# Kernel optimization log

Measured on AMD Instinct MI355X. Metric: run time of the kernel, lower is better.

## Reference

```python
import jax, jax.numpy as jnp
import numpy as np

N_CELLS_PER_SIDE = 16
MAX_K = 32
N_HEADS = 8
CHUNK = 128

_NEIGHBOR_OFFSETS = jnp.array([[-1, -1], [-1, 0], [-1, 1], [0, -1], [0, 0], [0, 1], [1, -1], [1, 0], [1, 1]], dtype=jnp.int32)


def cell_lookup(query_pos, cell_map, pos_min, pos_range):
    B, S, _ = query_pos.shape
    mpc = cell_map.shape[1]
    normalized = (query_pos - pos_min) / pos_range
    cell_xy = jnp.clip((normalized * N_CELLS_PER_SIDE).astype(jnp.int32), 0, N_CELLS_PER_SIDE - 1)
    nb = jnp.clip(cell_xy[:, :, None, :] + _NEIGHBOR_OFFSETS[None, None, :, :], 0, N_CELLS_PER_SIDE - 1)
    nidx = nb[..., 0] * N_CELLS_PER_SIDE + nb[..., 1]
    cand = cell_map[nidx].reshape(B, S, 9 * mpc)
    valid = cand >= 0
    return jnp.where(valid, cand, 0), valid


def threshold_gate(scores, tau, max_k):
    raw = scores - tau
    gate = jnp.where(raw > 0, raw, 1e-8 * jnp.exp(raw))
    eg = jnp.exp(gate) - 1.0
    k = min(max_k, scores.shape[-1])
    tv, _ = jax.lax.top_k(eg, k)
    eg = jnp.where(eg >= tv[:, :, -1:], eg, 0.0)
    gs = eg.sum(axis=-1, keepdims=True) + 1e-8
    strength = jnp.tanh(eg.max(axis=-1, keepdims=True))
    return eg / gs * strength


def setup_inputs() -> dict:
    key = jax.random.key(0)
    ks = jax.random.split(key, 16)
    B, S, D, N, P = 2, 1024, 512, 4096, 2
    n_cells, mpc = N_CELLS_PER_SIDE ** 2, 32
    return {
        "x": jax.random.normal(ks[0], (B, S, D), jnp.float32),
        "qk_pos": jax.random.uniform(ks[1], (B, S, P), jnp.float32),
        "v_pos": jax.random.uniform(ks[2], (B, S, P), jnp.float32),
        "tau_Q": jax.random.uniform(ks[3], (B, S, 1), jnp.float32),
        "tau_K": jax.random.uniform(ks[4], (B, S, 1), jnp.float32),
        "tau_V": jax.random.uniform(ks[5], (B, S, 1), jnp.float32),
        "qk_neurons": jax.random.normal(ks[6], (N, D), jnp.float32) / np.float32(np.sqrt(D)),
        "v_neurons": jax.random.normal(ks[7], (N, D), jnp.float32) / np.float32(np.sqrt(D)),
        "npos_qk": jax.random.uniform(ks[8], (N, P), jnp.float32),
        "npos_v": jax.random.uniform(ks[9], (N, P), jnp.float32),
        "cell_map_qk": jax.random.randint(ks[10], (n_cells, mpc), 0, N, jnp.int32),
        "cell_map_v": jax.random.randint(ks[11], (n_cells, mpc), 0, N, jnp.int32),
        "pos_min": jnp.zeros((P,), jnp.float32),
        "pos_range": jnp.ones((P,), jnp.float32),
        "expand_O": jax.random.normal(ks[12], (D, D), jnp.float32) * 0.02,
    }


def reference(x, qk_pos, v_pos, tau_Q, tau_K, tau_V, qk_neurons, v_neurons, npos_qk, npos_v, cell_map_qk, cell_map_v, pos_min, pos_range, expand_O):
    B, S, D = x.shape
    # full-sequence spatial cell lookup (small int tensors)
    ci_qk, m_qk = cell_lookup(qk_pos, cell_map_qk, pos_min, pos_range)
    ci_v, m_v = cell_lookup(v_pos, cell_map_v, pos_min, pos_range)
    ci_qk = jax.lax.stop_gradient(ci_qk)
    ci_v = jax.lax.stop_gradient(ci_v)
    nc = S // CHUNK  # S chosen divisible by CHUNK (no padding path needed)

    def chunks(a):
        return a.reshape(B, nc, CHUNK, *a.shape[2:]).swapaxes(0, 1)

    inp = tuple(map(chunks, (x, qk_pos, v_pos, tau_Q, tau_K, tau_V, ci_qk, m_qk, ci_v, m_v)))

    def step(carry, c):
        x_c, qkp, vp, tq, tk, tv, i_qk, mk, i_v, mv = c
        cand_qk = qk_neurons[i_qk]  # [B,C,n_cand,D]
        cand_v = v_neurons[i_v]
        act_qk = jnp.einsum('bsd,bsnd->bsn', x_c, cand_qk)
        act_v = jnp.einsum('bsd,bsnd->bsn', x_c, cand_v)
        s_qk = jnp.where(mk, act_qk, -1e9)
        s_v = jnp.where(mv, act_v, -1e9)
        gQ = threshold_gate(s_qk, tq, MAX_K)
        gK = threshold_gate(s_qk, tk, MAX_K)
        gV = threshold_gate(s_v, tv, MAX_K)
        Q_c = jnp.einsum('bsn,bsnd->bsd', act_qk * gQ * mk, cand_qk)
        K_c = jnp.einsum('bsn,bsnd->bsd', act_qk * gK * mk, cand_qk)
        V_c = jnp.einsum('bsn,bsnd->bsd', act_v * gV * mv, cand_v)
        pd_qk = jnp.sum((qkp[:, :, None, :] - npos_qk[i_qk]) ** 2, axis=-1)
        pl_qk = (jax.lax.stop_gradient(gQ) * pd_qk * mk).sum() / (mk.sum() + 1e-8)
        pd_v = jnp.sum((vp[:, :, None, :] - npos_v[i_v]) ** 2, axis=-1)
        pl_v = (jax.lax.stop_gradient(gV) * pd_v * mv).sum() / (mv.sum() + 1e-8)
        return carry, (Q_c, K_c, V_c, pl_qk + pl_v)

    _, (Qs, Ks, Vs, pls) = jax.lax.scan(step, 0, inp)

    def merge(a):
        return a.swapaxes(0, 1).reshape(B, S, D)

    Q, K, V = merge(Qs), merge(Ks), merge(Vs)
    pos_loss = pls.mean()  # == sum / n_chunks

    dh = D // N_HEADS
    Qh = Q.reshape(B, S, N_HEADS, dh).transpose(0, 2, 1, 3)
    Kh = K.reshape(B, S, N_HEADS, dh).transpose(0, 2, 1, 3)
    Vh = V.reshape(B, S, N_HEADS, dh).transpose(0, 2, 1, 3)
    scores = jnp.einsum('bhsd,bhtd->bhst', Qh, Kh) / jnp.sqrt(jnp.float32(dh))
    causal = jnp.tril(jnp.ones((S, S), dtype=jnp.bool_))
    scores = jnp.where(causal, scores, jnp.finfo(scores.dtype).min)
    attn = jax.nn.softmax(scores, axis=-1)
    out = jnp.einsum('bhst,bhtd->bhsd', attn, Vh)
    out = out.transpose(0, 2, 1, 3).reshape(B, S, D)
    out = out @ expand_O
    return out, pos_loss
```

## Files before the change

### kernel.cpp

```cpp
#include <hip/hip_runtime.h>
#include <math.h>

#define B_ 2
#define S_ 1024
#define D_ 512
#define N_ 4096
#define H_ 8
#define DH_ 64
#define NCAND 288
#define TOPK 32
#define NTOK (B_*S_)
#define NG8 512

#define NROWS 16384
#define NSLOT_BH 8704
#define NSLOTS (16*NSLOT_BH)

__device__ __forceinline__ float wave_sum(float v) {
    #pragma unroll
    for (int o = 32; o; o >>= 1) v += __shfl_xor(v, o);
    return v;
}
__device__ __forceinline__ float wave_max(float v) {
    #pragma unroll
    for (int o = 32; o; o >>= 1) v = fmaxf(v, __shfl_xor(v, o));
    return v;
}
__device__ __forceinline__ void fma4(float4& a, float s, const float4 b) {
    a.x += s * b.x; a.y += s * b.y; a.z += s * b.z; a.w += s * b.w;
}

__global__ __launch_bounds__(1024) void sort_tokens_kernel(
    const float* __restrict__ qk_pos, const float* __restrict__ v_pos,
    const float* __restrict__ pos_min, const float* __restrict__ pos_range,
    int* __restrict__ order_qk, int* __restrict__ order_v,
    int2* __restrict__ desc_qk, int2* __restrict__ desc_v)
{
    __shared__ int hist[256], tmp[256], offs[256], startc[256], gcnt[256];
    const int t = threadIdx.x;
    const int pass = blockIdx.x;
    const float pm0 = pos_min[0], pm1 = pos_min[1];
    const float pr0 = pos_range[0], pr1 = pos_range[1];
    const float* pos = pass ? v_pos : qk_pos;
    int* order = pass ? order_v : order_qk;
    int2* desc = pass ? desc_v : desc_qk;
    if (t < NG8) desc[t] = make_int2(0, 0);
    if (t < 256) hist[t] = 0;
    __syncthreads();
    int cell[2];
    #pragma unroll
    for (int k = 0; k < 2; k++) {
        int tok = t + k * 1024;
        float p0 = pos[tok * 2], p1 = pos[tok * 2 + 1];
        int cx = min(max((int)((p0 - pm0) / pr0 * 16.f), 0), 15);
        int cy = min(max((int)((p1 - pm1) / pr1 * 16.f), 0), 15);
        cell[k] = cx * 16 + cy;
        atomicAdd(&hist[cell[k]], 1);
    }
    __syncthreads();
    if (t < 256) tmp[t] = hist[t];
    __syncthreads();
    for (int d = 1; d < 256; d <<= 1) {
        int v = 0;
        if (t < 256 && t >= d) v = tmp[t - d];
        __syncthreads();
        if (t < 256) tmp[t] += v;
        __syncthreads();
    }
    if (t < 256) {
        startc[t] = tmp[t] - hist[t];
        offs[t]   = startc[t];
        gcnt[t]   = (hist[t] + 7) >> 3;
    }
    __syncthreads();
    #pragma unroll
    for (int k = 0; k < 2; k++) {
        int tok = t + k * 1024;
        int p = atomicAdd(&offs[cell[k]], 1);
        order[p] = tok;
    }
    __syncthreads();
    if (t < 256) tmp[t] = gcnt[t];
    __syncthreads();
    for (int d = 1; d < 256; d <<= 1) {
        int v = 0;
        if (t < 256 && t >= d) v = tmp[t - d];
        __syncthreads();
        if (t < 256) tmp[t] += v;
        __syncthreads();
    }
    if (t < 256) {
        int g0 = tmp[t] - gcnt[t];
        for (int k = 0; k < gcnt[t]; k++)
            desc[g0 + k] = make_int2(startc[t] + 8 * k, min(8, hist[t] - 8 * k));
    }
}

__device__ __forceinline__ int rank_topk(const float* __restrict__ actRow,
                                         int* __restrict__ ciRow, int lane) {
    unsigned ej[5];
    #pragma unroll
    for (int k = 0; k < 5; k++) {
        int j = lane + 64 * k;
        float f = (j < NCAND) ? actRow[j] : -1e30f;
        unsigned uu = __float_as_uint(f);
        ej[k] = (uu & 0x80000000u) ? ~uu : (uu | 0x80000000u);
    }
    unsigned T = 0u;
    for (int bit = 31; bit >= 0; bit--) {
        const unsigned cand = T | (1u << bit);
        int c = 0;
        #pragma unroll
        for (int k = 0; k < 5; k++)
            c += __popcll(__ballot(ej[k] >= cand));
        if (c >= TOPK) T = cand;
    }
    int base = 0;
    const unsigned long long below = (lane == 0) ? 0ull : (~0ull >> (64 - lane));
    #pragma unroll
    for (int k = 0; k < 5; k++) {
        const unsigned long long mk2 = __ballot(ej[k] >= T);
        if (ej[k] >= T) {
            int pos = base + __popcll(mk2 & below);
            ciRow[pos] = lane + 64 * k;
        }
        base += __popcll(mk2);
    }
    return base;
}

__global__ __launch_bounds__(256) void qkv_fused(
    const int2* __restrict__ desc_qk, const int* __restrict__ order_qk,
    const int2* __restrict__ desc_v,  const int* __restrict__ order_v,
    const float* __restrict__ x,
    const float* __restrict__ qk_pos, const float* __restrict__ v_pos,
    const float* __restrict__ tauQ, const float* __restrict__ tauK,
    const float* __restrict__ tauV,
    const float* __restrict__ qk_neurons, const float* __restrict__ v_neurons,
    const float* __restrict__ npos_qk, const float* __restrict__ npos_v,
    const int* __restrict__ cm_qk, const int* __restrict__ cm_v,
    const float* __restrict__ pos_min, const float* __restrict__ pos_range,
    float* __restrict__ Q, float* __restrict__ K, float* __restrict__ V,
    float* __restrict__ posacc)
{
    const int bid = blockIdx.x;
    const int role = bid & 1;
    const int gid = bid >> 1;
    const int2 dsc = role ? desc_v[gid] : desc_qk[gid];
    const int gstart = dsc.x, count = dsc.y;
    if (count == 0) return;

    const int*   order   = role ? order_v   : order_qk;
    const float* pose    = role ? v_pos     : qk_pos;
    const float* neurons = role ? v_neurons : qk_neurons;
    const float* npos    = role ? npos_v    : npos_qk;
    const int*   cmap    = role ? cm_v      : cm_qk;

    __shared__ int   idx[NCAND];
    __shared__ float msk[NCAND];
    __shared__ float act[8][NCAND];
    __shared__ int   ci[8][NCAND];
    __shared__ float cw1[8][NCAND], cw2[8][NCAND];
    __shared__ int   toks[8];

    const int t = threadIdx.x, wid = t >> 6, lane = t & 63;
    const int sub = lane & 15, grp = lane >> 4;
    if (t < 8) toks[t] = order[gstart + min(t, count - 1)];
    __syncthreads();
    const int token0 = toks[0];

    const float pm0 = pos_min[0], pm1 = pos_min[1];
    const float pr0 = pos_range[0], pr1 = pos_range[1];
    {
        const float p0 = pose[token0 * 2], p1 = pose[token0 * 2 + 1];
        const int cx = min(max((int)((p0 - pm0) / pr0 * 16.f), 0), 15);
        const int cy = min(max((int)((p1 - pm1) / pr1 * 16.f), 0), 15);
        for (int c = t; c < NCAND; c += 256) {
            int o = c >> 5, ms = c & 31;
            int nx = min(max(cx + o / 3 - 1, 0), 15), ny = min(max(cy + o % 3 - 1, 0), 15);
            int cand = cmap[(nx * 16 + ny) * 32 + ms];
            idx[c] = cand >= 0 ? cand : 0;
            msk[c] = cand >= 0 ? 1.f : 0.f;
        }
    }
    __syncthreads();

    const int tokA = 2 * grp, tokB = 2 * grp + 1;
    float4 xr0[8], xr1[8];
    {
        const float4* xp0 = (const float4*)(x + (size_t)toks[tokA] * D_);
        const float4* xp1 = (const float4*)(x + (size_t)toks[tokB] * D_);
        #pragma unroll
        for (int k = 0; k < 8; k++) {
            xr0[k] = xp0[k * 16 + sub];
            xr1[k] = xp1[k * 16 + sub];
        }
    }

    #define LOADROW(buf, c) do { \
        const float4* rp_ = (const float4*)(neurons + (size_t)idx[c] * D_); \
        _Pragma("unroll") \
        for (int k_ = 0; k_ < 8; k_++) buf[k_] = rp_[k_ * 16 + sub]; \
    } while (0)
    #define DOTSTORE(buf, c) do { \
        float f0_ = 0.f, f1_ = 0.f; \
        _Pragma("unroll") \
        for (int k_ = 0; k_ < 8; k_++) { \
            f0_ += xr0[k_].x*buf[k_].x + xr0[k_].y*buf[k_].y + xr0[k_].z*buf[k_].z + xr0[k_].w*buf[k_].w; \
            f1_ += xr1[k_].x*buf[k_].x + xr1[k_].y*buf[k_].y + xr1[k_].z*buf[k_].z + xr1[k_].w*buf[k_].w; \
        } \
        _Pragma("unroll") \
        for (int o_ = 1; o_ <= 8; o_ <<= 1) { \
            f0_ += __shfl_xor(f0_, o_); \
            f1_ += __shfl_xor(f1_, o_); \
        } \
        if (sub == 0) { \
            const float mv_ = msk[c]; \
            act[tokA][c] = (mv_ != 0.f) ? f0_ : -1e9f; \
            act[tokB][c] = (mv_ != 0.f) ? f1_ : -1e9f; \
        } \
    } while (0)

    {
        const int cb = wid * 72;
        float4 bufA[8], bufB[8];
        LOADROW(bufA, cb);
        for (int u = 0; u < 72; u += 2) {
            LOADROW(bufB, cb + u + 1);
            DOTSTORE(bufA, cb + u);
            if (u + 2 < 72) LOADROW(bufA, cb + u + 2);
            DOTSTORE(bufB, cb + u + 1);
        }
    }
    __syncthreads();

    float cmv = 0.f;
    for (int c = lane; c < NCAND; c += 64) cmv += msk[c];
    const float cm = wave_sum(cmv);

    int n0 = 0, n1 = 0;
    if (2 * wid < count)     n0 = rank_topk(act[2 * wid],     ci[2 * wid],     lane);
    if (2 * wid + 1 < count) n1 = rank_topk(act[2 * wid + 1], ci[2 * wid + 1], lane);

    if (role == 0) {
        #pragma unroll
        for (int i = 0; i < 2; i++) {
            const int tk = 2 * wid + i;
            if (tk >= count) continue;
            const int n = i ? n1 : n0;
            const int token = toks[tk];
            const float tq = tauQ[token], tkk = tauK[token];
            float sQ = 0.f, sK = 0.f, mQ = 0.f, mK = 0.f;
            for (int p = lane; p < n; p += 64) {
                float s = act[tk][ci[tk][p]];
                float rq = s - tq;
                float gq = (rq > 0.f) ? rq : 1e-8f * __expf(rq);
                float egq = __expf(gq) - 1.f;
                float rk = s - tkk;
                float gk = (rk > 0.f) ? rk : 1e-8f * __expf(rk);
                float egk = __expf(gk) - 1.f;
                cw1[tk][p] = egq; cw2[tk][p] = egk;
                sQ += egq; sK += egk;
                mQ = fmaxf(mQ, egq); mK = fmaxf(mK, egk);
            }
            sQ = wave_sum(sQ); mQ = wave_max(mQ);
            sK = wave_sum(sK); mK = wave_max(mK);
            const float scQ = tanhf(mQ) / (sQ + 1e-8f);
            const float scK = tanhf(mK) / (sK + 1e-8f);

            const float qp0 = pose[token * 2], qp1 = pose[token * 2 + 1];
            float plq = 0.f;
            for (int p = lane; p < n; p += 64) {
                int e = ci[tk][p];
                int id = idx[e];
                float m = msk[e], a = act[tk][e];
                float gq = cw1[tk][p] * scQ;
                cw1[tk][p] = a * gq * m;
                cw2[tk][p] = a * cw2[tk][p] * scK * m;
                ci[tk][p] = id;
                float d0 = qp0 - npos[id * 2], d1 = qp1 - npos[id * 2 + 1];
                plq += gq * (d0 * d0 + d1 * d1) * m;
            }
            plq = wave_sum(plq);
            if (lane == 0) {
                int chunk = (token & 1023) >> 7;
                atomicAdd(&posacc[chunk], plq);
                atomicAdd(&posacc[8 + chunk], cm);
            }

            float4 qa0 = {0,0,0,0}, qa1 = {0,0,0,0};
            float4 ka0 = {0,0,0,0}, ka1 = {0,0,0,0};
            int p = 0;
            for (; p + 1 < n; p += 2) {
                const float* rA = neurons + (size_t)ci[tk][p] * D_ + lane * 8;
                const float* rB = neurons + (size_t)ci[tk][p + 1] * D_ + lane * 8;
                const float4 A0 = *(const float4*)rA;
                const float4 A1 = *(const float4*)(rA + 4);
                const float4 B0 = *(const float4*)rB;
                const float4 B1 = *(const float4*)(rB + 4);
                const float wA = cw1[tk][p], bA = cw2[tk][p];
                const float wB = cw1[tk][p + 1], bB = cw2[tk][p + 1];
                fma4(qa0, wA, A0); fma4(qa0, wB, B0);
                fma4(qa1, wA, A1); fma4(qa1, wB, B1);
                fma4(ka0, bA, A0); fma4(ka0, bB, B0);
                fma4(ka1, bA, A1); fma4(ka1, bB, B1);
            }
            if (p < n) {
                const float* rA = neurons + (size_t)ci[tk][p] * D_ + lane * 8;
                const float4 A0 = *(const float4*)rA;
                const float4 A1 = *(const float4*)(rA + 4);
                const float wA = cw1[tk][p], bA = cw2[tk][p];
                fma4(qa0, wA, A0); fma4(qa1, wA, A1);
                fma4(ka0, bA, A0); fma4(ka1, bA, A1);
            }
            *(float4*)(Q + (size_t)token * D_ + lane * 8)     = qa0;
            *(float4*)(Q + (size_t)token * D_ + lane * 8 + 4) = qa1;
            *(float4*)(K + (size_t)token * D_ + lane * 8)     = ka0;
            *(float4*)(K + (size_t)token * D_ + lane * 8 + 4) = ka1;
        }
    } else {
        #pragma unroll
        for (int i = 0; i < 2; i++) {
            const int tk = 2 * wid + i;
            if (tk >= count) continue;
            const int n = i ? n1 : n0;
            const int token = toks[tk];
            const float tv = tauV[token];
            float sV = 0.f, mV = 0.f;
            for (int p = lane; p < n; p += 64) {
                float s = act[tk][ci[tk][p]];
                float rv = s - tv;
                float gv = (rv > 0.f) ? rv : 1e-8f * __expf(rv);
                float egv = __expf(gv) - 1.f;
                cw1[tk][p] = egv;
                sV += egv; mV = fmaxf(mV, egv);
            }
            sV = wave_sum(sV); mV = wave_max(mV);
            const float scV = tanhf(mV) / (sV + 1e-8f);

            const float vp0 = pose[token * 2], vp1 = pose[token * 2 + 1];
            float plv = 0.f;
            for (int p = lane; p < n; p += 64) {
                int e = ci[tk][p];
                int id = idx[e];
                float m = msk[e], a = act[tk][e];
                float gv = cw1[tk][p] * scV;
                cw1[tk][p] = a * gv * m;
                ci[tk][p] = id;
                float d0 = vp0 - npos[id * 2], d1 = vp1 - npos[id * 2 + 1];
                plv += gv * (d0 * d0 + d1 * d1) * m;
            }
            plv = wave_sum(plv);
            if (lane == 0) {
                int chunk = (token & 1023) >> 7;
                atomicAdd(&posacc[16 + chunk], plv);
                atomicAdd(&posacc[24 + chunk], cm);
            }

            float4 va0 = {0,0,0,0}, va1 = {0,0,0,0};
            int p = 0;
            for (; p + 1 < n; p += 2) {
                const float* rA = neurons + (size_t)ci[tk][p] * D_ + lane * 8;
                const float* rB = neurons + (size_t)ci[tk][p + 1] * D_ + lane * 8;
                const float4 A0 = *(const float4*)rA;
                const float4 A1 = *(const float4*)(rA + 4);
                const float4 B0 = *(const float4*)rB;
                const float4 B1 = *(const float4*)(rB + 4);
                const float wA = cw1[tk][p], wB = cw1[tk][p + 1];
                fma4(va0, wA, A0); fma4(va0, wB, B0);
                fma4(va1, wA, A1); fma4(va1, wB, B1);
            }
            if (p < n) {
                const float* rA = neurons + (size_t)ci[tk][p] * D_ + lane * 8;
                const float4 A0 = *(const float4*)rA;
                const float4 A1 = *(const float4*)(rA + 4);
                const float wA = cw1[tk][p];
                fma4(va0, wA, A0); fma4(va1, wA, A1);
            }
            *(float4*)(V + (size_t)token * D_ + lane * 8)     = va0;
            *(float4*)(V + (size_t)token * D_ + lane * 8 + 4) = va1;
        }
    }
}

typedef __attribute__((ext_vector_type(8))) short short8;
typedef __attribute__((ext_vector_type(4))) float f32x4;

__device__ __forceinline__ ushort f2b_rn(float f) {
    unsigned u = __float_as_uint(f);
    return (ushort)((u + 0x7FFFu + ((u >> 16) & 1u)) >> 16);
}
__device__ __forceinline__ float b2f(ushort h) {
    return __uint_as_float(((unsigned)h) << 16);
}
__device__ __forceinline__ int swzi(int row, int c8) {
    return row * 64 + ((c8 ^ (row & 7)) << 3);
}

__global__ __launch_bounds__(256, 2) void attn_partial_kernel(
    const float* __restrict__ Q, const float* __restrict__ K,
    const float* __restrict__ V,
    float* __restrict__ pm, float* __restrict__ pl, float* __restrict__ po)
{
    const int xx = blockIdx.x & 7;
    int kq = blockIdx.x >> 3;
    const int bh = xx + 8 * (kq >= 72);
    kq = (kq >= 72) ? kq - 72 : kq;
    int rblk = 0;
    while (kq >= 2 * (rblk + 1)) { kq -= 2 * (rblk + 1); rblk++; }
    const int sp = kq;
    const int b = bh >> 3, h = bh & 7;
    const int j0 = sp * 64;
    const int rbase = rblk * 128;

    __shared__ __align__(16) ushort sKhi[64 * 64], sKlo[64 * 64];
    __shared__ __align__(16) ushort sVthi[64 * 64], sVtlo[64 * 64];
    __shared__ __align__(16) float sPool[8192];

    const int t = threadIdx.x;
    const int w = t >> 6, lane = t & 63;
    const int g = lane >> 4, ln = lane & 15;

    {
        const int srow = t >> 2, scol = (t & 3) << 4;
        const float* Kg = K + ((size_t)(b * S_ + j0 + srow)) * D_ + h * DH_ + scol;
        const float* Vg = V + ((size_t)(b * S_ + j0 + srow)) * D_ + h * DH_ + scol;
        union { float4 f4[4]; float f[16]; } kf, vf;
        kf.f4[0] = *(const float4*)(Kg);
        kf.f4[1] = *(const float4*)(Kg + 4);
        kf.f4[2] = *(const float4*)(Kg + 8);
        kf.f4[3] = *(const float4*)(Kg + 12);
        vf.f4[0] = *(const float4*)(Vg);
        vf.f4[1] = *(const float4*)(Vg + 4);
        vf.f4[2] = *(const float4*)(Vg + 8);
        vf.f4[3] = *(const float4*)(Vg + 12);
        union { uint4 d[2]; ushort u[16]; } uh, ul;
        #pragma unroll
        for (int i = 0; i < 16; i++) {
            uh.u[i] = f2b_rn(kf.f[i]);
            ul.u[i] = f2b_rn(kf.f[i] - b2f(uh.u[i]));
        }
        const int c8 = (t & 3) << 1;
        *(uint4*)&sKhi[swzi(srow, c8)]     = uh.d[0];
        *(uint4*)&sKhi[swzi(srow, c8 + 1)] = uh.d[1];
        *(uint4*)&sKlo[swzi(srow, c8)]     = ul.d[0];
        *(uint4*)&sKlo[swzi(srow, c8 + 1)] = ul.d[1];
        #pragma unroll
        for (int i = 0; i < 16; i++) sPool[srow * 65 + scol + i] = vf.f[i];
    }
    __syncthreads();
    {
        const int drow = t >> 2, kcol = (t & 3) << 4;
        union { uint4 d[2]; ushort u[16]; } uh, ul;
        #pragma unroll
        for (int i = 0; i < 16; i++) {
            const float f = sPool[(kcol + i) * 65 + drow];
            uh.u[i] = f2b_rn(f);
            ul.u[i] = f2b_rn(f - b2f(uh.u[i]));
        }
        const int c8 = (t & 3) << 1;
        *(uint4*)&sVthi[swzi(drow, c8)]     = uh.d[0];
        *(uint4*)&sVthi[swzi(drow, c8 + 1)] = uh.d[1];
        *(uint4*)&sVtlo[swzi(drow, c8)]     = ul.d[0];
        *(uint4*)&sVtlo[swzi(drow, c8 + 1)] = ul.d[1];
    }
    __syncthreads();

    const int wrow = rbase + w * 32;
    if (wrow + 31 < j0) return;

    ushort* sPw = (ushort*)sPool + w * 4096;

    short8 qhi[2][2], qlo[2][2];
    #pragma unroll
    for (int qt = 0; qt < 2; qt++) {
        const int qrow = wrow + qt * 16 + ln;
        const float* Qg = Q + ((size_t)(b * S_ + qrow)) * D_ + h * DH_ + g * 8;
        #pragma unroll
        for (int ds = 0; ds < 2; ds++) {
            union { float4 f4[2]; float f[8]; } qf;
            qf.f4[0] = *(const float4*)(Qg + ds * 32);
            qf.f4[1] = *(const float4*)(Qg + ds * 32 + 4);
            union { short8 v; ushort u[8]; } uh, ul;
            #pragma unroll
            for (int i = 0; i < 8; i++) {
                uh.u[i] = f2b_rn(qf.f[i]);
                ul.u[i] = f2b_rn(qf.f[i] - b2f(uh.u[i]));
            }
            qhi[qt][ds] = uh.v; qlo[qt][ds] = ul.v;
        }
    }

    const f32x4 fzero = {0.f, 0.f, 0.f, 0.f};
    f32x4 sT[2][4];
    #pragma unroll
    for (int qt = 0; qt < 2; qt++)
        #pragma unroll
        for (int kt = 0; kt < 4; kt++)
            sT[qt][kt] = fzero;
    #pragma unroll
    for (int ds = 0; ds < 2; ds++) {
        #pragma unroll
        for (int kt = 0; kt < 4; kt++) {
            const int krow = kt * 16 + ln;
            const short8 khi = *(const short8*)&sKhi[swzi(krow, ds * 4 + g)];
            const short8 klo = *(const short8*)&sKlo[swzi(krow, ds * 4 + g)];
            #pragma unroll
            for (int qt = 0; qt < 2; qt++) {
                sT[qt][kt] = __builtin_amdgcn_mfma_f32_16x16x32_bf16(khi, qhi[qt][ds], sT[qt][kt], 0, 0, 0);
                sT[qt][kt] = __builtin_amdgcn_mfma_f32_16x16x32_bf16(khi, qlo[qt][ds], sT[qt][kt], 0, 0, 0);
                sT[qt][kt] = __builtin_amdgcn_mfma_f32_16x16x32_bf16(klo, qhi[qt][ds], sT[qt][kt], 0, 0, 0);
            }
        }
    }

    #pragma unroll
    for (int qt = 0; qt < 2; qt++) {
        const int qg = wrow + qt * 16 + ln;
        float pv[16];
        float mq = -1e30f;
        #pragma unroll
        for (int kt = 0; kt < 4; kt++)
            #pragma unroll
            for (int r = 0; r < 4; r++) {
                const int kg = j0 + kt * 16 + g * 4 + r;
                float s = sT[qt][kt][r] * 0.125f;
                s = (kg <= qg) ? s : -1e30f;
                pv[kt * 4 + r] = s;
                mq = fmaxf(mq, s);
            }
        mq = fmaxf(mq, __shfl_xor(mq, 16));
        mq = fmaxf(mq, __shfl_xor(mq, 32));
        const float base = (mq < -1e29f) ? 0.f : mq;
        float lq = 0.f;
        #pragma unroll
        for (int i = 0; i < 16; i++) {
            const float e = __expf(pv[i] - base);
            pv[i] = e;
            lq += e;
        }
        lq += __shfl_xor(lq, 16);
        lq += __shfl_xor(lq, 32);

        const int qrow = qt * 16 + ln;
        #pragma unroll
        for (int kt = 0; kt < 4; kt++) {
            union { uint2 d; ushort u[4]; } h4, l4;
            #pragma unroll
            for (int r = 0; r < 4; r++) {
                const float f = pv[kt * 4 + r];
                h4.u[r] = f2b_rn(f);
                l4.u[r] = f2b_rn(f - b2f(h4.u[r]));
            }
            const int c8 = kt * 2 + (g >> 1);
            const int idx = qrow * 64 + ((c8 ^ (qrow & 7)) << 3) + ((g & 1) << 2);
            *(uint2*)&sPw[idx] = h4.d;
            *(uint2*)&sPw[2048 + idx] = l4.d;
        }
        if (g == 0 && qg >= j0) {
            const int gr = qg >> 6;
            const size_t slot = (size_t)bh * NSLOT_BH + 32 * gr * (gr + 1)
                              + (size_t)(qg & 63) * (gr + 1) + sp;
            pm[slot] = mq; pl[slot] = lq;
        }
    }

    f32x4 ot[4][2];
    #pragma unroll
    for (int dt = 0; dt < 4; dt++)
        #pragma unroll
        for (int qt = 0; qt < 2; qt++)
            ot[dt][qt] = fzero;
    #pragma unroll
    for (int ks = 0; ks < 2; ks++) {
        short8 pfh[2], pfl[2];
        #pragma unroll
        for (int qt = 0; qt < 2; qt++) {
            const int qrow = qt * 16 + ln;
            const int idx = qrow * 64 + (((ks * 4 + g) ^ (qrow & 7)) << 3);
            pfh[qt] = *(const short8*)&sPw[idx];
            pfl[qt] = *(const short8*)&sPw[2048 + idx];
        }
        #pragma unroll
        for (int dt = 0; dt < 4; dt++) {
            const int drow = dt * 16 + ln;
            const short8 vh = *(const short8*)&sVthi[swzi(drow, ks * 4 + g)];
            const short8 vl = *(const short8*)&sVtlo[swzi(drow, ks * 4 + g)];
            #pragma unroll
            for (int qt = 0; qt < 2; qt++) {
                ot[dt][qt] = __builtin_amdgcn_mfma_f32_16x16x32_bf16(vh, pfh[qt], ot[dt][qt], 0, 0, 0);
                ot[dt][qt] = __builtin_amdgcn_mfma_f32_16x16x32_bf16(vh, pfl[qt], ot[dt][qt], 0, 0, 0);
                ot[dt][qt] = __builtin_amdgcn_mfma_f32_16x16x32_bf16(vl, pfh[qt], ot[dt][qt], 0, 0, 0);
            }
        }
    }

    #pragma unroll
    for (int qt = 0; qt < 2; qt++) {
        const int qg = wrow + qt * 16 + ln;
        if (qg < j0) continue;
        const int gr = qg >> 6;
        const size_t slot = (size_t)bh * NSLOT_BH + 32 * gr * (gr + 1)
                          + (size_t)(qg & 63) * (gr + 1) + sp;
        float* od = po + slot * 64 + g * 4;
        #pragma unroll
        for (int dt = 0; dt < 4; dt++)
            *(f32x4*)(od + dt * 16) = ot[dt][qt];
    }
}

__global__ __launch_bounds__(256) void attn_combine_kernel(
    const float* __restrict__ pm, const float* __restrict__ pl,
    const float* __restrict__ po, float* __restrict__ AO)
{
    const int gth = blockIdx.x * 256 + threadIdx.x;
    const int r = gth >> 6, d = gth & 63;
    const int i = r & 1023, bh = r >> 10;
    const int b = bh >> 3, h = bh & 7;
    const int g = i >> 6;
    const int ns = g + 1;
    const size_t slot0 = (size_t)bh * NSLOT_BH + 32 * g * (g + 1)
                       + (size_t)(i & 63) * (g + 1);
    float mstar = -INFINITY, lstar = 0.f, ostar = 0.f;
    for (int s = 0; s < ns; s++) {
        const float mi = pm[slot0 + s];
        const float nm = fmaxf(mstar, mi);
        const float a = __expf(mstar - nm);
        const float w = __expf(mi - nm);
        lstar = lstar * a + pl[slot0 + s] * w;
        ostar = ostar * a + po[(slot0 + s) * 64 + d] * w;
        mstar = nm;
    }
    AO[((size_t)(b * S_ + i)) * D_ + h * DH_ + d] = ostar / lstar;
}

__global__ __launch_bounds__(256) void proj_kernel(
    const float* __restrict__ A, const float* __restrict__ W,
    float* __restrict__ out)
{
    __shared__ float rows[4][D_];
    const int blk = blockIdx.x;
    const int t = threadIdx.x;
    {
        const float4* af = (const float4*)(A + (size_t)blk * 4 * D_);
        float4* rf = (float4*)&rows[0][0];
        rf[t] = af[t]; rf[t + 256] = af[t + 256];
    }
    __syncthreads();
    float acc0[4] = {0,0,0,0}, acc1[4] = {0,0,0,0};
    for (int d = 0; d < D_; d += 4) {
        float r0[4], r1[4], r2[4], r3[4];
        *(float4*)r0 = *(const float4*)&rows[0][d];
        *(float4*)r1 = *(const float4*)&rows[1][d];
        *(float4*)r2 = *(const float4*)&rows[2][d];
        *(float4*)r3 = *(const float4*)&rows[3][d];
        #pragma unroll
        for (int j = 0; j < 4; j++) {
            float w0 = W[(size_t)(d + j) * D_ + t];
            float w1 = W[(size_t)(d + j) * D_ + t + 256];
            acc0[0] += r0[j] * w0; acc1[0] += r0[j] * w1;
            acc0[1] += r1[j] * w0; acc1[1] += r1[j] * w1;
            acc0[2] += r2[j] * w0; acc1[2] += r2[j] * w1;
            acc0[3] += r3[j] * w0; acc1[3] += r3[j] * w1;
        }
    }
    #pragma unroll
    for (int k = 0; k < 4; k++) {
        const size_t base = (size_t)(blk * 4 + k) * D_;
        out[base + t] = acc0[k];
        out[base + t + 256] = acc1[k];
    }
}

__global__ void zero_acc_kernel(float* acc) {
    if (threadIdx.x < 32) acc[threadIdx.x] = 0.f;
}
__global__ void ploss_kernel(const float* __restrict__ acc, float* __restrict__ out) {
    float ssum = 0.f;
    for (int c = 0; c < 8; c++) {
        ssum += acc[c]      / (acc[8 + c]  + 1e-8f);
        ssum += acc[16 + c] / (acc[24 + c] + 1e-8f);
    }
    out[0] = ssum * 0.125f;
}

extern "C" void kernel_launch(void* const* d_in, const int* in_sizes, int n_in,
                              void* d_out, int out_size, void* d_ws, size_t ws_size,
                              hipStream_t stream) {
    const float* x          = (const float*)d_in[0];
    const float* qk_pos     = (const float*)d_in[1];
    const float* v_pos      = (const float*)d_in[2];
    const float* tauQ       = (const float*)d_in[3];
    const float* tauK       = (const float*)d_in[4];
    const float* tauV       = (const float*)d_in[5];
    const float* qk_neurons = (const float*)d_in[6];
    const float* v_neurons  = (const float*)d_in[7];
    const float* npos_qk    = (const float*)d_in[8];
    const float* npos_v     = (const float*)d_in[9];
    const int*   cm_qk      = (const int*)d_in[10];
    const int*   cm_v       = (const int*)d_in[11];
    const float* pos_min    = (const float*)d_in[12];
    const float* pos_range  = (const float*)d_in[13];
    const float* expand_O   = (const float*)d_in[14];

    float* ws = (float*)d_ws;
    const size_t TDf = (size_t)NTOK * D_;
    float* Q   = ws;
    float* K   = ws + TDf;
    float* V   = ws + 2 * TDf;
    float* AO  = ws + 3 * TDf;
    float* acc = ws + 4 * TDf;
    int*   order_qk = (int*)(ws + 4 * TDf + 64);
    int*   order_v  = order_qk + NTOK;
    int2*  desc_qk  = (int2*)(order_v + NTOK);
    int2*  desc_v   = desc_qk + NG8;
    const size_t head = 4 * TDf + 64 + 2 * NTOK + 4 * NG8;

    float* pm = ws + head;
    float* pl = pm + (size_t)NSLOTS;
    float* po = pl + (size_t)NSLOTS;

    float* out = (float*)d_out;

    zero_acc_kernel<<<1, 64, 0, stream>>>(acc);
    sort_tokens_kernel<<<2, 1024, 0, stream>>>(qk_pos, v_pos, pos_min, pos_range,
                                               order_qk, order_v, desc_qk, desc_v);
    qkv_fused<<<2 * NG8, 256, 0, stream>>>(desc_qk, order_qk, desc_v, order_v,
                                           x, qk_pos, v_pos, tauQ, tauK, tauV,
                                           qk_neurons, v_neurons, npos_qk, npos_v,
                                           cm_qk, cm_v, pos_min, pos_range,
                                           Q, K, V, acc);
    attn_partial_kernel<<<1152, 256, 0, stream>>>(Q, K, V, pm, pl, po);
    attn_combine_kernel<<<(NROWS * 64) / 256, 256, 0, stream>>>(pm, pl, po, AO);
    proj_kernel<<<NTOK / 4, 256, 0, stream>>>(AO, expand_O, out);
    ploss_kernel<<<1, 1, 0, stream>>>(acc, out + TDf);
}
```

Measured before the change: 286.5 us.

## Use 512-thread blocks in qkv_fused with one wave per token

Doubles the qkv_fused block from 4 to 8 waves. Each wave now scores 36 candidate rows instead of 72 and handles a single token's top-k, gating and gather instead of two. It also swizzles block IDs and pads the shared arrays to 296 entries, likely to reduce bank conflicts. The aim is more parallelism and latency hiding in the gather-heavy phase, at the cost of larger blocks that may lower occupancy or leave waves idle when a group has fewer than 8 tokens.

```diff
diff --git a/kernel.cpp b/kernel.cpp
--- a/kernel.cpp
+++ b/kernel.cpp
@@ -8,6 +8,7 @@
 #define H_ 8
 #define DH_ 64
 #define NCAND 288
+#define NCP 296
 #define TOPK 32
 #define NTOK (B_*S_)
 #define NG8 512
@@ -129,7 +130,7 @@
     return base;
 }
 
-__global__ __launch_bounds__(256) void qkv_fused(
+__global__ __launch_bounds__(512) void qkv_fused(
     const int2* __restrict__ desc_qk, const int* __restrict__ order_qk,
     const int2* __restrict__ desc_v,  const int* __restrict__ order_v,
     const float* __restrict__ x,
@@ -143,9 +144,10 @@
     float* __restrict__ Q, float* __restrict__ K, float* __restrict__ V,
     float* __restrict__ posacc)
 {
-    const int bid = blockIdx.x;
-    const int role = bid & 1;
-    const int gid = bid >> 1;
+    const int bid0 = blockIdx.x;
+    const int swz = ((bid0 & 7) << 7) | (bid0 >> 3);
+    const int role = swz & 1;
+    const int gid = swz >> 1;
     const int2 dsc = role ? desc_v[gid] : desc_qk[gid];
     const int gstart = dsc.x, count = dsc.y;
     if (count == 0) return;
@@ -158,9 +160,9 @@
 
     __shared__ int   idx[NCAND];
     __shared__ float msk[NCAND];
-    __shared__ float act[8][NCAND];
-    __shared__ int   ci[8][NCAND];
-    __shared__ float cw1[8][NCAND], cw2[8][NCAND];
+    __shared__ float act[8][NCP];
+    __shared__ int   ci[8][NCP];
+    __shared__ float cw1[8][NCP], cw2[8][NCP];
     __shared__ int   toks[8];
 
     const int t = threadIdx.x, wid = t >> 6, lane = t & 63;
@@ -175,7 +177,7 @@
         const float p0 = pose[token0 * 2], p1 = pose[token0 * 2 + 1];
         const int cx = min(max((int)((p0 - pm0) / pr0 * 16.f), 0), 15);
         const int cy = min(max((int)((p1 - pm1) / pr1 * 16.f), 0), 15);
-        for (int c = t; c < NCAND; c += 256) {
+        for (int c = t; c < NCAND; c += 512) {
             int o = c >> 5, ms = c & 31;
             int nx = min(max(cx + o / 3 - 1, 0), 15), ny = min(max(cy + o % 3 - 1, 0), 15);
             int cand = cmap[(nx * 16 + ny) * 32 + ms];
@@ -222,164 +224,151 @@
     } while (0)
 
     {
-        const int cb = wid * 72;
+        const int cb = wid * 36;
         float4 bufA[8], bufB[8];
         LOADROW(bufA, cb);
-        for (int u = 0; u < 72; u += 2) {
+        for (int u = 0; u < 36; u += 2) {
             LOADROW(bufB, cb + u + 1);
             DOTSTORE(bufA, cb + u);
-            if (u + 2 < 72) LOADROW(bufA, cb + u + 2);
+            if (u + 2 < 36) LOADROW(bufA, cb + u + 2);
             DOTSTORE(bufB, cb + u + 1);
         }
     }
     __syncthreads();
+    const int tk = wid;
+    if (tk >= count) return;
 
     float cmv = 0.f;
     for (int c = lane; c < NCAND; c += 64) cmv += msk[c];
     const float cm = wave_sum(cmv);
 
-    int n0 = 0, n1 = 0;
-    if (2 * wid < count)     n0 = rank_topk(act[2 * wid],     ci[2 * wid],     lane);
-    if (2 * wid + 1 < count) n1 = rank_topk(act[2 * wid + 1], ci[2 * wid + 1], lane);
+    const int n = rank_topk(act[tk], ci[tk], lane);
+    const int token = toks[tk];
 
     if (role == 0) {
-        #pragma unroll
-        for (int i = 0; i < 2; i++) {
-            const int tk = 2 * wid + i;
-            if (tk >= count) continue;
-            const int n = i ? n1 : n0;
-            const int token = toks[tk];
-            const float tq = tauQ[token], tkk = tauK[token];
-            float sQ = 0.f, sK = 0.f, mQ = 0.f, mK = 0.f;
-            for (int p = lane; p < n; p += 64) {
-                float s = act[tk][ci[tk][p]];
-                float rq = s - tq;
-                float gq = (rq > 0.f) ? rq : 1e-8f * __expf(rq);
-                float egq = __expf(gq) - 1.f;
-                float rk = s - tkk;
-                float gk = (rk > 0.f) ? rk : 1e-8f * __expf(rk);
-                float egk = __expf(gk) - 1.f;
-                cw1[tk][p] = egq; cw2[tk][p] = egk;
-                sQ += egq; sK += egk;
-                mQ = fmaxf(mQ, egq); mK = fmaxf(mK, egk);
-            }
-            sQ = wave_sum(sQ); mQ = wave_max(mQ);
-            sK = wave_sum(sK); mK = wave_max(mK);
-            const float scQ = tanhf(mQ) / (sQ + 1e-8f);
-            const float scK = tanhf(mK) / (sK + 1e-8f);
-
-            const float qp0 = pose[token * 2], qp1 = pose[token * 2 + 1];
-            float plq = 0.f;
-            for (int p = lane; p < n; p += 64) {
-                int e = ci[tk][p];
-                int id = idx[e];
-                float m = msk[e], a = act[tk][e];
-                float gq = cw1[tk][p] * scQ;
-                cw1[tk][p] = a * gq * m;
-                cw2[tk][p] = a * cw2[tk][p] * scK * m;
-                ci[tk][p] = id;
-                float d0 = qp0 - npos[id * 2], d1 = qp1 - npos[id * 2 + 1];
-                plq += gq * (d0 * d0 + d1 * d1) * m;
-            }
-            plq = wave_sum(plq);
-            if (lane == 0) {
-                int chunk = (token & 1023) >> 7;
-                atomicAdd(&posacc[chunk], plq);
-                atomicAdd(&posacc[8 + chunk], cm);
-            }
-
-            float4 qa0 = {0,0,0,0}, qa1 = {0,0,0,0};
-            float4 ka0 = {0,0,0,0}, ka1 = {0,0,0,0};
-            int p = 0;
-            for (; p + 1 < n; p += 2) {
-                const float* rA = neurons + (size_t)ci[tk][p] * D_ + lane * 8;
-                const float* rB = neurons + (size_t)ci[tk][p + 1] * D_ + lane * 8;
-                const float4 A0 = *(const float4*)rA;
-                const float4 A1 = *(const float4*)(rA + 4);
-                const float4 B0 = *(const float4*)rB;
-                const float4 B1 = *(const float4*)(rB + 4);
-                const float wA = cw1[tk][p], bA = cw2[tk][p];
-                const float wB = cw1[tk][p + 1], bB = cw2[tk][p + 1];
-                fma4(qa0, wA, A0); fma4(qa0, wB, B0);
-                fma4(qa1, wA, A1); fma4(qa1, wB, B1);
-                fma4(ka0, bA, A0); fma4(ka0, bB, B0);
-                fma4(ka1, bA, A1); fma4(ka1, bB, B1);
-            }
-            if (p < n) {
-                const float* rA = neurons + (size_t)ci[tk][p] * D_ + lane * 8;
-                const float4 A0 = *(const float4*)rA;
-                const float4 A1 = *(const float4*)(rA + 4);
-                const float wA = cw1[tk][p], bA = cw2[tk][p];
-                fma4(qa0, wA, A0); fma4(qa1, wA, A1);
-                fma4(ka0, bA, A0); fma4(ka1, bA, A1);
-            }
-            *(float4*)(Q + (size_t)token * D_ + lane * 8)     = qa0;
-            *(float4*)(Q + (size_t)token * D_ + lane * 8 + 4) = qa1;
-            *(float4*)(K + (size_t)token * D_ + lane * 8)     = ka0;
-            *(float4*)(K + (size_t)token * D_ + lane * 8 + 4) = ka1;
-        }
+        const float tq = tauQ[token], tkk = tauK[token];
+        float sQ = 0.f, sK = 0.f, mQ = 0.f, mK = 0.f;
+        for (int p = lane; p < n; p += 64) {
+            float s = act[tk][ci[tk][p]];
+            float rq = s - tq;
+            float gq = (rq > 0.f) ? rq : 1e-8f * __expf(rq);
+            float egq = __expf(gq) - 1.f;
+            float rk = s - tkk;
+            float gk = (rk > 0.f) ? rk : 1e-8f * __expf(rk);
+            float egk = __expf(gk) - 1.f;
+            cw1[tk][p] = egq; cw2[tk][p] = egk;
+            sQ += egq; sK += egk;
+            mQ = fmaxf(mQ, egq); mK = fmaxf(mK, egk);
+        }
+        sQ = wave_sum(sQ); mQ = wave_max(mQ);
+        sK = wave_sum(sK); mK = wave_max(mK);
+        const float scQ = tanhf(mQ) / (sQ + 1e-8f);
+        const float scK = tanhf(mK) / (sK + 1e-8f);
+
+        const float qp0 = pose[token * 2], qp1 = pose[token * 2 + 1];
+        float plq = 0.f;
+        for (int p = lane; p < n; p += 64) {
+            int e = ci[tk][p];
+            int id = idx[e];
+            float m = msk[e], a = act[tk][e];
+            float gq = cw1[tk][p] * scQ;
+            cw1[tk][p] = a * gq * m;
+            cw2[tk][p] = a * cw2[tk][p] * scK * m;
+            ci[tk][p] = id;
+            float d0 = qp0 - npos[id * 2], d1 = qp1 - npos[id * 2 + 1];
+            plq += gq * (d0 * d0 + d1 * d1) * m;
+        }
+        plq = wave_sum(plq);
+        if (lane == 0) {
+            int chunk = (token & 1023) >> 7;
+            atomicAdd(&posacc[chunk], plq);
+            atomicAdd(&posacc[8 + chunk], cm);
+        }
+
+        float4 qa0 = {0,0,0,0}, qa1 = {0,0,0,0};
+        float4 ka0 = {0,0,0,0}, ka1 = {0,0,0,0};
+        int p = 0;
+        for (; p + 1 < n; p += 2) {
+            const float* rA = neurons + (size_t)ci[tk][p] * D_ + lane * 8;
+            const float* rB = neurons + (size_t)ci[tk][p + 1] * D_ + lane * 8;
+            const float4 A0 = *(const float4*)rA;
+            const float4 A1 = *(const float4*)(rA + 4);
+            const float4 B0 = *(const float4*)rB;
+            const float4 B1 = *(const float4*)(rB + 4);
+            const float wA = cw1[tk][p], bA = cw2[tk][p];
+            const float wB = cw1[tk][p + 1], bB = cw2[tk][p + 1];
+            fma4(qa0, wA, A0); fma4(qa0, wB, B0);
+            fma4(qa1, wA, A1); fma4(qa1, wB, B1);
+            fma4(ka0, bA, A0); fma4(ka0, bB, B0);
+            fma4(ka1, bA, A1); fma4(ka1, bB, B1);
+        }
+        if (p < n) {
+            const float* rA = neurons + (size_t)ci[tk][p] * D_ + lane * 8;
+            const float4 A0 = *(const float4*)rA;
+            const float4 A1 = *(const float4*)(rA + 4);
+            const float wA = cw1[tk][p], bA = cw2[tk][p];
+            fma4(qa0, wA, A0); fma4(qa1, wA, A1);
+            fma4(ka0, bA, A0); fma4(ka1, bA, A1);
+        }
+        *(float4*)(Q + (size_t)token * D_ + lane * 8)     = qa0;
+        *(float4*)(Q + (size_t)token * D_ + lane * 8 + 4) = qa1;
+        *(float4*)(K + (size_t)token * D_ + lane * 8)     = ka0;
+        *(float4*)(K + (size_t)token * D_ + lane * 8 + 4) = ka1;
     } else {
-        #pragma unroll
-        for (int i = 0; i < 2; i++) {
-            const int tk = 2 * wid + i;
-            if (tk >= count) continue;
-            const int n = i ? n1 : n0;
-            const int token = toks[tk];
-            const float tv = tauV[token];
-            float sV = 0.f, mV = 0.f;
-            for (int p = lane; p < n; p += 64) {
-                float s = act[tk][ci[tk][p]];
-                float rv = s - tv;
-                float gv = (rv > 0.f) ? rv : 1e-8f * __expf(rv);
-                float egv = __expf(gv) - 1.f;
-                cw1[tk][p] = egv;
-                sV += egv; mV = fmaxf(mV, egv);
-            }
-            sV = wave_sum(sV); mV = wave_max(mV);
-            const float scV = tanhf(mV) / (sV + 1e-8f);
-
-            const float vp0 = pose[token * 2], vp1 = pose[token * 2 + 1];
-            float plv = 0.f;
-            for (int p = lane; p < n; p += 64) {
-                int e = ci[tk][p];
-                int id = idx[e];
-                float m = msk[e], a = act[tk][e];
-                float gv = cw1[tk][p] * scV;
-                cw1[tk][p] = a * gv * m;
-                ci[tk][p] = id;
-                float d0 = vp0 - npos[id * 2], d1 = vp1 - npos[id * 2 + 1];
-                plv += gv * (d0 * d0 + d1 * d1) * m;
-            }
-            plv = wave_sum(plv);
-            if (lane == 0) {
-                int chunk = (token & 1023) >> 7;
-                atomicAdd(&posacc[16 + chunk], plv);
-                atomicAdd(&posacc[24 + chunk], cm);
-            }
-
-            float4 va0 = {0,0,0,0}, va1 = {0,0,0,0};
-            int p = 0;
-            for (; p + 1 < n; p += 2) {
-                const float* rA = neurons + (size_t)ci[tk][p] * D_ + lane * 8;
-                const float* rB = neurons + (size_t)ci[tk][p + 1] * D_ + lane * 8;
-                const float4 A0 = *(const float4*)rA;
-                const float4 A1 = *(const float4*)(rA + 4);
-                const float4 B0 = *(const float4*)rB;
-                const float4 B1 = *(const float4*)(rB + 4);
-                const float wA = cw1[tk][p], wB = cw1[tk][p + 1];
-                fma4(va0, wA, A0); fma4(va0, wB, B0);
-                fma4(va1, wA, A1); fma4(va1, wB, B1);
-            }
-            if (p < n) {
-                const float* rA = neurons + (size_t)ci[tk][p] * D_ + lane * 8;
-                const float4 A0 = *(const float4*)rA;
-                const float4 A1 = *(const float4*)(rA + 4);
-                const float wA = cw1[tk][p];
-                fma4(va0, wA, A0); fma4(va1, wA, A1);
-            }
-            *(float4*)(V + (size_t)token * D_ + lane * 8)     = va0;
-            *(float4*)(V + (size_t)token * D_ + lane * 8 + 4) = va1;
-        }
+        const float tv = tauV[token];
+        float sV = 0.f, mV = 0.f;
+        for (int p = lane; p < n; p += 64) {
+            float s = act[tk][ci[tk][p]];
+            float rv = s - tv;
+            float gv = (rv > 0.f) ? rv : 1e-8f * __expf(rv);
+            float egv = __expf(gv) - 1.f;
+            cw1[tk][p] = egv;
+            sV += egv; mV = fmaxf(mV, egv);
+        }
+        sV = wave_sum(sV); mV = wave_max(mV);
+        const float scV = tanhf(mV) / (sV + 1e-8f);
+
+        const float vp0 = pose[token * 2], vp1 = pose[token * 2 + 1];
+        float plv = 0.f;
+        for (int p = lane; p < n; p += 64) {
+            int e = ci[tk][p];
+            int id = idx[e];
+            float m = msk[e], a = act[tk][e];
+            float gv = cw1[tk][p] * scV;
+            cw1[tk][p] = a * gv * m;
+            ci[tk][p] = id;
+            float d0 = vp0 - npos[id * 2], d1 = vp1 - npos[id * 2 + 1];
+            plv += gv * (d0 * d0 + d1 * d1) * m;
+        }
+        plv = wave_sum(plv);
+        if (lane == 0) {
+            int chunk = (token & 1023) >> 7;
+            atomicAdd(&posacc[16 + chunk], plv);
+            atomicAdd(&posacc[24 + chunk], cm);
+        }
+
+        float4 va0 = {0,0,0,0}, va1 = {0,0,0,0};
+        int p = 0;
+        for (; p + 1 < n; p += 2) {
+            const float* rA = neurons + (size_t)ci[tk][p] * D_ + lane * 8;
+            const float* rB = neurons + (size_t)ci[tk][p + 1] * D_ + lane * 8;
+            const float4 A0 = *(const float4*)rA;
+            const float4 A1 = *(const float4*)(rA + 4);
+            const float4 B0 = *(const float4*)rB;
+            const float4 B1 = *(const float4*)(rB + 4);
+            const float wA = cw1[tk][p], wB = cw1[tk][p + 1];
+            fma4(va0, wA, A0); fma4(va0, wB, B0);
+            fma4(va1, wA, A1); fma4(va1, wB, B1);
+        }
+        if (p < n) {
+            const float* rA = neurons + (size_t)ci[tk][p] * D_ + lane * 8;
+            const float4 A0 = *(const float4*)rA;
+            const float4 A1 = *(const float4*)(rA + 4);
+            const float wA = cw1[tk][p];
+            fma4(va0, wA, A0); fma4(va1, wA, A1);
+        }
+        *(float4*)(V + (size_t)token * D_ + lane * 8)     = va0;
+        *(float4*)(V + (size_t)token * D_ + lane * 8 + 4) = va1;
     }
 }
 
@@ -725,7 +714,7 @@
     zero_acc_kernel<<<1, 64, 0, stream>>>(acc);
     sort_tokens_kernel<<<2, 1024, 0, stream>>>(qk_pos, v_pos, pos_min, pos_range,
                                                order_qk, order_v, desc_qk, desc_v);
-    qkv_fused<<<2 * NG8, 256, 0, stream>>>(desc_qk, order_qk, desc_v, order_v,
+    qkv_fused<<<2 * NG8, 512, 0, stream>>>(desc_qk, order_qk, desc_v, order_v,
                                            x, qk_pos, v_pos, tauQ, tauK, tauV,
                                            qk_neurons, v_neurons, npos_qk, npos_v,
                                            cm_qk, cm_v, pos_min, pos_range,
```

After: 317.8 us. 1.11x slower.
